# Optimization experiments

Measured on AMD Instinct MI355X. Metric: run time of the kernel, lower is better.

## Reference

```python
import jax, jax.numpy as jnp
import numpy as np
from jax import lax

EPS = 1e-5
KV_DOWN = 4

def _bn(z, g, b, m, v):
    # eval-mode BatchNorm2d over channel axis 1
    inv = (g / jnp.sqrt(v + EPS))[None, :, None, None]
    return z * inv + (b - m * g / jnp.sqrt(v + EPS))[None, :, None, None]

def setup_inputs() -> dict:
    key = jax.random.key(0)
    ks = jax.random.split(key, 8)
    B, C, H, W = 8, 256, 128, 128
    AC, VC = 64, 128
    return {
        "x": jax.random.normal(ks[0], (B, C, H, W), jnp.float32),
        "wq": jax.random.normal(ks[1], (AC, C), jnp.float32) * 0.05,
        "wk": jax.random.normal(ks[2], (AC, C), jnp.float32) * 0.05,
        "wv": jax.random.normal(ks[3], (VC, C), jnp.float32) * 0.05,
        "wproj": jax.random.normal(ks[4], (C, VC), jnp.float32) * 0.05,
        "bn_g": jnp.ones((C,), jnp.float32),
        "bn_b": jnp.zeros((C,), jnp.float32),
        "bn_m": jax.random.normal(ks[5], (C,), jnp.float32) * 0.1,
        "bn_v": jax.random.uniform(ks[5], (C,), jnp.float32, 0.5, 1.5),
        "dw_w": jax.random.normal(ks[6], (C, 1, 3, 3), jnp.float32) * 0.1,
        "pw_w": jax.random.normal(ks[7], (C, C), jnp.float32) * 0.05,
        "mbn_g": jnp.ones((C,), jnp.float32),
        "mbn_b": jnp.zeros((C,), jnp.float32),
        "mbn_m": jax.random.normal(ks[7], (C,), jnp.float32) * 0.1,
        "mbn_v": jax.random.uniform(ks[6], (C,), jnp.float32, 0.5, 1.5),
    }

def reference(x, wq, wk, wv, wproj, bn_g, bn_b, bn_m, bn_v, dw_w, pw_w, mbn_g, mbn_b, mbn_m, mbn_v):
    b, c, h, w = x.shape
    d = KV_DOWN
    scale = wq.shape[0] ** -0.5
    # Q from full-res x via 1x1 conv
    q = jnp.einsum('ac,bchw->bahw', wq, x)            # [B,AC,H,W]
    # avg-pool x for K,V
    x_kv = x.reshape(b, c, h // d, d, w // d, d).mean(axis=(3, 5))
    k = jnp.einsum('ac,bchw->bahw', wk, x_kv)          # [B,AC,H',W']
    v = jnp.einsum('vc,bchw->bvhw', wv, x_kv)          # [B,VC,H',W']
    N = h * w
    M = (h // d) * (w // d)
    qf = q.reshape(b, -1, N)                           # [B,AC,N]
    kf = k.reshape(b, -1, M)                           # [B,AC,M]
    vf = v.reshape(b, -1, M)                           # [B,VC,M]
    attn = jnp.einsum('ban,bam->bnm', qf, kf) * scale  # [B,N,M]
    attn = jax.nn.softmax(attn, axis=-1)
    y = jnp.einsum('bnm,bvm->bvn', attn, vf)           # [B,VC,N]
    y = y.reshape(b, vf.shape[1], h, w)
    y = jnp.einsum('cv,bvhw->bchw', wproj, y)          # proj -> [B,C,H,W]
    y = jax.nn.silu(_bn(y, bn_g, bn_b, bn_m, bn_v))
    # depthwise 3x3 + pointwise 1x1 mix
    z = lax.conv_general_dilated(y, dw_w, (1, 1), 'SAME',
                                 dimension_numbers=('NCHW', 'OIHW', 'NCHW'),
                                 feature_group_count=c)
    z = jnp.einsum('oc,bchw->bohw', pw_w, z)
    z = _bn(z, mbn_g, mbn_b, mbn_m, mbn_v)
    return x + jax.nn.silu(z)
```

## Files before the change

kernel.cpp:

```cpp
#include <hip/hip_runtime.h>
#include <hip/hip_bf16.h>
#include <math.h>

#define EPSV 1e-5f

typedef short bf16x8 __attribute__((ext_vector_type(8)));
typedef float f32x16 __attribute__((ext_vector_type(16)));
typedef unsigned int uint4v __attribute__((ext_vector_type(4)));

__device__ __forceinline__ float silu_f(float v) { return v / (1.0f + __expf(-v)); }

__device__ __forceinline__ unsigned short f2bf(float f) {
  __hip_bfloat16 h = __float2bfloat16(f);
  return __builtin_bit_cast(unsigned short, h);
}

__device__ __forceinline__ float fexp2(float x) {
  float r;
  asm("v_exp_f32 %0, %1" : "=v"(r) : "v"(x));
  return r;
}

__device__ __forceinline__ unsigned int cvtpk(float lo, float hi) {
  unsigned int r;
  asm("v_cvt_pk_bf16_f32 %0, %1, %2" : "=v"(r) : "v"(lo), "v"(hi));
  return r;
}

__device__ __forceinline__ bf16x8 ld_frag(const unsigned short* p) {
  return *reinterpret_cast<const bf16x8*>(p);
}

__device__ __forceinline__ void gload16(const unsigned short* g, unsigned short* l) {
  __builtin_amdgcn_global_load_lds((const __attribute__((address_space(1))) void*)g,
                                   (__attribute__((address_space(3))) void*)l, 16, 0, 0);
}

__global__ __launch_bounds__(256) void pool_kernel(const float* __restrict__ x,
                                                   float* __restrict__ xkv) {
  int idx = blockIdx.x * 256 + threadIdx.x;
  int m = idx & 1023, bc = idx >> 10;
  int hh = m >> 5, ww = m & 31;
  const float* base = x + ((size_t)bc << 14) + (size_t)(hh * 4) * 128 + ww * 4;
  float s = 0.f;
#pragma unroll
  for (int i = 0; i < 4; ++i) {
    float4 v = *reinterpret_cast<const float4*>(base + i * 128);
    s += v.x + v.y + v.z + v.w;
  }
  xkv[idx] = s * 0.0625f;
}

__global__ __launch_bounds__(256) void cvtT_kernel(const float* __restrict__ x,
                                                   unsigned short* __restrict__ xbfT) {
  __shared__ unsigned short sT[64 * 68];
  const int tid = threadIdx.x;
  const int b = blockIdx.z, c0 = blockIdx.y * 64, n0 = blockIdx.x * 64;
  const float* xs = x + ((size_t)(b * 256 + c0) << 14) + n0;
#pragma unroll
  for (int pass = 0; pass < 4; ++pass) {
    int cc = (tid >> 4) + pass * 16;
    int col = (tid & 15) * 4;
    float4 v = *reinterpret_cast<const float4*>(xs + ((size_t)cc << 14) + col);
    unsigned short* d = &sT[cc * 68 + col];
    d[0] = f2bf(v.x); d[1] = f2bf(v.y); d[2] = f2bf(v.z); d[3] = f2bf(v.w);
  }
  __syncthreads();
  int n = tid >> 2, cs = (tid & 3) * 16;
  unsigned short tmp[16];
#pragma unroll
  for (int i = 0; i < 16; ++i) tmp[i] = sT[(cs + i) * 68 + n];
  unsigned short* dst = xbfT + (((size_t)b * 16384 + n0 + n) << 8) + c0 + cs;
  *reinterpret_cast<uint4*>(dst) = *reinterpret_cast<uint4*>(tmp);
  *reinterpret_cast<uint4*>(dst + 8) = *reinterpret_cast<uint4*>(tmp + 8);
}

__global__ __launch_bounds__(256) void prep_kernel(const float* __restrict__ wproj,
                                                   const float* __restrict__ bng,
                                                   const float* __restrict__ bnb,
                                                   const float* __restrict__ bnm,
                                                   const float* __restrict__ bnv,
                                                   unsigned short* __restrict__ wpb,
                                                   float* __restrict__ bnsc,
                                                   float* __restrict__ bnsh) {
  int i = blockIdx.x * 256 + threadIdx.x;
  if (i < 32768) {
    int j = i & 7, lane = (i >> 3) & 63, kc = (i >> 9) & 7, ctcg = i >> 12;
    int row = (ctcg >> 2) * 128 + (ctcg & 3) * 32 + (lane & 31);
    int col = kc * 16 + (lane >> 5) * 8 + j;
    wpb[i] = f2bf(wproj[row * 128 + col]);
  } else if (i < 33024) {
    int c = i - 32768;
    float inv = bng[c] / sqrtf(bnv[c] + EPSV);
    bnsc[c] = inv;
    bnsh[c] = bnb[c] - bnm[c] * inv;
  }
}

__global__ __launch_bounds__(256) void prep_pw(const float* __restrict__ pww,
                                               const float* __restrict__ wq,
                                               unsigned short* __restrict__ pwPack,
                                               unsigned short* __restrict__ wqPack) {
  int f = blockIdx.x * 256 + threadIdx.x;
  if (f < 65536) {
    int j = f & 7, lane = (f >> 3) & 63, ks = (f >> 9) & 15, mt = f >> 13;
    int o = mt * 32 + (lane & 31);
    int cc = ks * 16 + (lane >> 5) * 8 + j;
    pwPack[f] = f2bf(pww[o * 256 + cc]);
  } else if (f < 81920) {
    int g = f - 65536;
    int j = g & 7, lane = (g >> 3) & 63, ks = (g >> 9) & 15, mt = g >> 13;
    int o = mt * 32 + (lane & 31);
    int cc = ks * 16 + (lane >> 5) * 8 + j;
    wqPack[g] = f2bf(wq[o * 256 + cc] * 0.18033688011112042f);
  }
}

__global__ __launch_bounds__(256, 4) void gemm_kv(const float* __restrict__ wk,
                                                  const float* __restrict__ wv,
                                                  const float* __restrict__ X,
                                                  unsigned short* __restrict__ Kt,
                                                  unsigned short* __restrict__ Vbf) {
  __shared__ float sW[64 * 68];
  __shared__ float sX[64 * 68];
  const int tid = threadIdx.x;
  const int n0 = blockIdx.x * 64;
  const int part = blockIdx.y;
  const int m0 = (part == 0) ? 0 : (part - 1) * 64;
  const float* W = (part == 0) ? wk : wv;
  const size_t xoff = (size_t)blockIdx.z * 256 * 1024;
  const int tm4 = (tid >> 4) * 4, tn4 = (tid & 15) * 4;
  float acc[4][4] = {};
  for (int k0 = 0; k0 < 256; k0 += 64) {
    __syncthreads();
#pragma unroll
    for (int i = 0; i < 16; ++i) {
      int flat = tid + i * 256;
      int kk = flat & 63, mm = flat >> 6;
      sW[kk * 68 + mm] = W[(m0 + mm) * 256 + k0 + kk];
      sX[kk * 68 + mm] = X[xoff + (size_t)(k0 + kk) * 1024 + n0 + mm];
    }
    __syncthreads();
#pragma unroll 8
    for (int k = 0; k < 64; ++k) {
      float4 a4 = *reinterpret_cast<const float4*>(&sW[k * 68 + tm4]);
      float4 b4 = *reinterpret_cast<const float4*>(&sX[k * 68 + tn4]);
      float av[4] = {a4.x, a4.y, a4.z, a4.w};
      float bv[4] = {b4.x, b4.y, b4.z, b4.w};
#pragma unroll
      for (int i = 0; i < 4; ++i)
#pragma unroll
        for (int j = 0; j < 4; ++j) acc[i][j] += av[i] * bv[j];
    }
  }
  if (part == 0) {
    const size_t coff = (size_t)blockIdx.z * 65536;
#pragma unroll
    for (int j = 0; j < 4; ++j) {
      ushort4 o;
      o.x = f2bf(acc[0][j]); o.y = f2bf(acc[1][j]);
      o.z = f2bf(acc[2][j]); o.w = f2bf(acc[3][j]);
      *reinterpret_cast<ushort4*>(&Kt[coff + (size_t)(n0 + tn4 + j) * 64 + tm4]) = o;
    }
  } else {
    const size_t coff = (size_t)blockIdx.z * 131072;
#pragma unroll
    for (int i = 0; i < 4; ++i) {
      ushort4 o;
      o.x = f2bf(acc[i][0]); o.y = f2bf(acc[i][1]);
      o.z = f2bf(acc[i][2]); o.w = f2bf(acc[i][3]);
      *reinterpret_cast<ushort4*>(&Vbf[coff + (size_t)(m0 + tm4 + i) * 1024 + n0 + tn4]) = o;
    }
  }
}

__global__ __launch_bounds__(256, 4) void qgemm_mfma(const unsigned short* __restrict__ xbfT,
                                                     const unsigned short* __restrict__ wqPack,
                                                     unsigned short* __restrict__ Qt) {
  __shared__ __align__(16) unsigned short sX[2][128 * 64];
  const int tid = threadIdx.x;
  const int w = tid >> 6, l = tid & 63;
  const int lq = l & 31, hi = l >> 5;
  const int b = blockIdx.y;
  const int n0 = blockIdx.x * 128;
  const int lr8 = l >> 3;
  const int gslot = (l & 7) ^ (lr8 & 7);
  const unsigned short* xb = xbfT + (((size_t)b * 16384 + n0) << 8);

#define QSTAGE(buf, ck)                                                       \
  {                                                                           \
    _Pragma("unroll") for (int i = 0; i < 4; ++i) {                           \
      int row = w * 32 + i * 8;                                               \
      gload16(xb + ((size_t)(row + lr8) << 8) + (ck) * 64 + gslot * 8,        \
              &sX[buf][row * 64]);                                            \
    }                                                                         \
  }

  f32x16 acc0, acc1;
#pragma unroll
  for (int i = 0; i < 16; ++i) { acc0[i] = 0.f; acc1[i] = 0.f; }

  QSTAGE(0, 0);
  __syncthreads();
  int cur = 0;
  for (int ck = 0; ck < 4; ++ck) {
    if (ck < 3) QSTAGE(cur ^ 1, ck + 1);
    const unsigned short* xl = sX[cur];
#pragma unroll
    for (int k2 = 0; k2 < 4; ++k2) {
      bf16x8 bfr = ld_frag(xl + (w * 32 + lq) * 64 + (((2 * k2 + hi) ^ (lq & 7)) << 3));
      int ks = ck * 4 + k2;
      bf16x8 a0 = ld_frag(wqPack + (size_t)((ks)*64 + l) * 8);
      bf16x8 a1 = ld_frag(wqPack + (size_t)((16 + ks) * 64 + l) * 8);
      acc0 = __builtin_amdgcn_mfma_f32_32x32x16_bf16(a0, bfr, acc0, 0, 0, 0);
      acc1 = __builtin_amdgcn_mfma_f32_32x32x16_bf16(a1, bfr, acc1, 0, 0, 0);
    }
    __syncthreads();
    cur ^= 1;
  }
#undef QSTAGE

  unsigned short* so2 = (unsigned short*)sX + w * 2304;
#pragma unroll
  for (int r = 0; r < 16; ++r) {
    int a = (r & 3) + 8 * (r >> 2) + 4 * hi;
    so2[lq * 72 + a] = f2bf(acc0[r]);
    so2[lq * 72 + 32 + a] = f2bf(acc1[r]);
  }
#pragma unroll
  for (int pass = 0; pass < 4; ++pass) {
    int flat = pass * 64 + l;
    int row = flat >> 3, col8 = (flat & 7) * 8;
    bf16x8 v = ld_frag(so2 + row * 72 + col8);
    *reinterpret_cast<bf16x8*>(Qt + ((size_t)b * 16384 + n0 + w * 32 + row) * 64 + col8) = v;
  }
}

__global__ __launch_bounds__(256, 3) void attn_mfma(
    const unsigned short* __restrict__ Qt, const unsigned short* __restrict__ Kt,
    const unsigned short* __restrict__ Vb, const unsigned short* __restrict__ wpb,
    const float* __restrict__ bnsc, const float* __restrict__ bnsh,
    unsigned short* __restrict__ yact) {
  __shared__ __align__(16) unsigned char smem[49152];
  unsigned short* const sK = (unsigned short*)smem;
  unsigned short* const sV = (unsigned short*)(smem + 16384);
  const int tid = threadIdx.x;
  const int w = tid >> 6, l = tid & 63;
  const int lq = l & 31, hi = l >> 5;
  const int bid = blockIdx.x;
  const int b = bid >> 7;
  const int q0 = (bid & 127) * 128 + w * 32;

  const unsigned short* Qp = Qt + ((size_t)b * 16384 + q0 + lq) * 64 + hi * 8;
  bf16x8 qf[4];
#pragma unroll
  for (int kc = 0; kc < 4; ++kc) qf[kc] = ld_frag(Qp + kc * 16);

  const uint4v ow = {0x3F803F80u, 0x3F803F80u, 0x3F803F80u, 0x3F803F80u};
  const bf16x8 onesf = __builtin_bit_cast(bf16x8, ow);

  f32x16 acc[4], accS;
#pragma unroll
  for (int t = 0; t < 4; ++t)
#pragma unroll
    for (int i = 0; i < 16; ++i) acc[t][i] = 0.f;
#pragma unroll
  for (int i = 0; i < 16; ++i) accS[i] = 0.f;

  const unsigned short* Kb = Kt + (size_t)b * 65536;
  const unsigned short* Vbb = Vb + (size_t)b * 131072;
  const int lr8 = l >> 3;
  const int gslot = (l & 7) ^ (lr8 & 7);

#define STAGE(buf, ch)                                                           \
  {                                                                              \
    const int m0s = (ch) * 64;                                                   \
    _Pragma("unroll") for (int i = 0; i < 2; ++i) {                              \
      int row8 = w * 16 + i * 8;                                                 \
      gload16(Kb + (size_t)(m0s + row8 + lr8) * 64 + gslot * 8,                  \
              sK + (buf) * 4096 + row8 * 64);                                    \
    }                                                                            \
    _Pragma("unroll") for (int j = 0; j < 4; ++j) {                              \
      int vc8 = w * 32 + j * 8;                                                  \
      gload16(Vbb + (size_t)(vc8 + lr8) * 1024 + m0s + gslot * 8,                \
              sV + (buf) * 8192 + vc8 * 64);                                     \
    }                                                                            \
  }

  STAGE(0, 0);
  __syncthreads();
  int cur = 0;
  for (int ch = 0; ch < 16; ++ch) {
    if (ch < 15) STAGE(cur ^ 1, ch + 1);
    const unsigned short* kb = sK + cur * 4096;
    const unsigned short* vb = sV + cur * 8192;
#pragma unroll
    for (int msi = 0; msi < 2; ++msi) {
      const int ms = msi * 32;
      bf16x8 kf[4];
#pragma unroll
      for (int kc = 0; kc < 4; ++kc)
        kf[kc] = ld_frag(kb + (ms + lq) * 64 + (((2 * kc + hi) ^ (lq & 7)) << 3));
      f32x16 sa;
#pragma unroll
      for (int i = 0; i < 16; ++i) sa[i] = 0.f;
      __builtin_amdgcn_s_setprio(1);
#pragma unroll
      for (int kc = 0; kc < 4; ++kc)
        sa = __builtin_amdgcn_mfma_f32_32x32x16_bf16(kf[kc], qf[kc], sa, 0, 0, 0);
      __builtin_amdgcn_s_setprio(0);

      float p[16];
#pragma unroll
      for (int r = 0; r < 16; ++r) p[r] = fexp2(sa[r] - 16.0f);

      unsigned int wpk[8];
#pragma unroll
      for (int i = 0; i < 8; ++i) wpk[i] = cvtpk(p[2 * i], p[2 * i + 1]);
      auto s01 = __builtin_amdgcn_permlane32_swap(wpk[0], wpk[2], false, false);
      auto s23 = __builtin_amdgcn_permlane32_swap(wpk[1], wpk[3], false, false);
      auto s45 = __builtin_amdgcn_permlane32_swap(wpk[4], wpk[6], false, false);
      auto s67 = __builtin_amdgcn_permlane32_swap(wpk[5], wpk[7], false, false);
      uint4v f0 = {(unsigned int)s01[0], (unsigned int)s23[0], (unsigned int)s01[1],
                   (unsigned int)s23[1]};
      uint4v f1 = {(unsigned int)s45[0], (unsigned int)s67[0], (unsigned int)s45[1],
                   (unsigned int)s67[1]};
      bf16x8 pf0 = __builtin_bit_cast(bf16x8, f0);
      bf16x8 pf1 = __builtin_bit_cast(bf16x8, f1);

      __builtin_amdgcn_s_setprio(1);
#pragma unroll
      for (int t = 0; t < 4; ++t) {
        bf16x8 vf0 =
            ld_frag(vb + (t * 32 + lq) * 64 + ((((ms >> 3) + hi) ^ (lq & 7)) << 3));
        bf16x8 vf1 =
            ld_frag(vb + (t * 32 + lq) * 64 + ((((ms >> 3) + 2 + hi) ^ (lq & 7)) << 3));
        acc[t] = __builtin_amdgcn_mfma_f32_32x32x16_bf16(pf0, vf0, acc[t], 0, 0, 0);
        acc[t] = __builtin_amdgcn_mfma_f32_32x32x16_bf16(pf1, vf1, acc[t], 0, 0, 0);
      }
      accS = __builtin_amdgcn_mfma_f32_32x32x16_bf16(pf0, onesf, accS, 0, 0, 0);
      accS = __builtin_amdgcn_mfma_f32_32x32x16_bf16(pf1, onesf, accS, 0, 0, 0);
      __builtin_amdgcn_s_setprio(0);
    }
    __syncthreads();
    cur ^= 1;
  }
#undef STAGE

  unsigned short* so = (unsigned short*)smem + w * 4096;
#pragma unroll
  for (int t = 0; t < 4; ++t)
#pragma unroll
    for (int r = 0; r < 16; ++r) {
      int q = (r & 3) + 8 * (r >> 2) + 4 * hi;
      int col = t * 32 + lq;
      so[q * 128 + (col ^ ((q & 15) << 3))] = f2bf(acc[t][r] / accS[r]);
    }
  __syncthreads();

  bf16x8 of[8];
#pragma unroll
  for (int kc = 0; kc < 8; ++kc) {
    int colr = kc * 16 + hi * 8;
    of[kc] = ld_frag(&so[lq * 128 + (colr ^ ((lq & 15) << 3))]);
  }
#pragma unroll
  for (int cg = 0; cg < 2; ++cg) {
    f32x16 z[4];
#pragma unroll
    for (int t = 0; t < 4; ++t)
#pragma unroll
      for (int i = 0; i < 16; ++i) z[t][i] = 0.f;
#pragma unroll
    for (int ct = 0; ct < 4; ++ct) {
      const unsigned short* wp = wpb + (size_t)(cg * 4 + ct) * 4096 + (size_t)l * 8;
#pragma unroll
      for (int kc = 0; kc < 8; ++kc) {
        bf16x8 wf = ld_frag(wp + kc * 512);
        z[ct] = __builtin_amdgcn_mfma_f32_32x32x16_bf16(wf, of[kc], z[ct], 0, 0, 0);
      }
    }
#pragma unroll
    for (int ct = 0; ct < 4; ++ct)
#pragma unroll
      for (int r = 0; r < 16; ++r) {
        int c = cg * 128 + ct * 32 + (r & 3) + 8 * (r >> 2) + 4 * hi;
        float val = z[ct][r] * bnsc[c] + bnsh[c];
        yact[((size_t)(b * 256 + c)) * 16384 + q0 + lq] = f2bf(silu_f(val));
      }
  }
}

__global__ __launch_bounds__(256, 4) void dwconv_kernel(const unsigned short* __restrict__ yact,
                                                        const float* __restrict__ dww,
                                                        unsigned short* __restrict__ D) {
  __shared__ unsigned int sP[130 * 67];
  const int tid = threadIdx.x;
  const int bc = blockIdx.x;
  const int c = bc & 255;
  for (int s = tid; s < 130 * 67; s += 256) sP[s] = 0;
  __syncthreads();
  const unsigned int* ysrc = reinterpret_cast<const unsigned int*>(yact) + (size_t)bc * 8192;
#pragma unroll
  for (int i = 0; i < 8; ++i) {
    int wi4 = tid + 256 * i;
    uint4 v = *reinterpret_cast<const uint4*>(ysrc + (size_t)wi4 * 4);
    int row = wi4 >> 4;
    int cw = (wi4 & 15) * 4;
    unsigned int* dst = &sP[(row + 1) * 67 + 1 + cw];
    dst[0] = v.x; dst[1] = v.y; dst[2] = v.z; dst[3] = v.w;
  }
  __syncthreads();
  float w9[9];
#pragma unroll
  for (int k = 0; k < 9; ++k) w9[k] = dww[c * 9 + k];
#pragma unroll
  for (int it = 0; it < 4; ++it) {
    int u = tid + 256 * it;
    int rho = u >> 4;
    int wg = u & 15;
    float a0[8] = {}, a1[8] = {};
#pragma unroll
    for (int ir = 0; ir < 4; ++ir) {
      int srow = rho * 2 + ir;
      const unsigned int* rp = &sP[srow * 67 + 4 * wg];
      float f[12];
#pragma unroll
      for (int k = 0; k < 6; ++k) {
        unsigned int wv = rp[k];
        f[2 * k] = __builtin_bit_cast(float, wv << 16);
        f[2 * k + 1] = __builtin_bit_cast(float, wv & 0xffff0000u);
      }
      if (ir < 3) {
#pragma unroll
        for (int cc = 0; cc < 8; ++cc)
#pragma unroll
          for (int dc = 0; dc < 3; ++dc) a0[cc] += f[cc + 1 + dc] * w9[ir * 3 + dc];
      }
      if (ir > 0) {
#pragma unroll
        for (int cc = 0; cc < 8; ++cc)
#pragma unroll
          for (int dc = 0; dc < 3; ++dc) a1[cc] += f[cc + 1 + dc] * w9[(ir - 1) * 3 + dc];
      }
    }
    uint4v o0, o1;
#pragma unroll
    for (int k = 0; k < 4; ++k) {
      o0[k] = (unsigned int)f2bf(a0[2 * k]) | ((unsigned int)f2bf(a0[2 * k + 1]) << 16);
      o1[k] = (unsigned int)f2bf(a1[2 * k]) | ((unsigned int)f2bf(a1[2 * k + 1]) << 16);
    }
    size_t ob = (size_t)bc * 8192 + (size_t)(rho * 2) * 64 + wg * 4;
    unsigned int* Dw = reinterpret_cast<unsigned int*>(D);
    *reinterpret_cast<uint4v*>(Dw + ob) = o0;
    *reinterpret_cast<uint4v*>(Dw + ob + 64) = o1;
  }
}

__global__ __launch_bounds__(256, 2) void pwmix_kernel(
    const unsigned short* __restrict__ D, const unsigned short* __restrict__ pwPack,
    const float* __restrict__ x, const float* __restrict__ mg,
    const float* __restrict__ mb2, const float* __restrict__ mmu,
    const float* __restrict__ mvv, float* __restrict__ out) {
  __shared__ unsigned int sDt[16384];
  __shared__ float smsc[256], smsh[256];
  const int tid = threadIdx.x;
  const int w = tid >> 6, l = tid & 63;
  const int lq = l & 31, hi = l >> 5;
  const int h = blockIdx.x, b = blockIdx.y;
  if (tid < 256) {
    float inv = mg[tid] * rsqrtf(mvv[tid] + EPSV);
    smsc[tid] = inv;
    smsh[tid] = mb2[tid] - mmu[tid] * inv;
  }
  const size_t dbase = ((size_t)b * 256) * 16384 + (size_t)h * 128;
#pragma unroll
  for (int i = 0; i < 8; ++i) {
    int cp = 64 * (i & 1) + 16 * w + (l >> 2);
    int pg = (l & 3) + 4 * (i >> 1);
    const unsigned short* g0 = D + dbase + (size_t)(cp * 2) * 16384 + pg * 8;
    bf16x8 d0 = ld_frag(g0);
    bf16x8 d1 = ld_frag(g0 + 16384);
#pragma unroll
    for (int j = 0; j < 8; ++j) {
      unsigned int word = ((unsigned int)(unsigned short)d0[j]) |
                          (((unsigned int)(unsigned short)d1[j]) << 16);
      int widx = ((pg * 8 + j) * 128 + cp) ^ (j << 2);
      sDt[widx] = word;
    }
  }
  __syncthreads();

  f32x16 z[2][4];
#pragma unroll
  for (int mti = 0; mti < 2; ++mti)
#pragma unroll
    for (int nt = 0; nt < 4; ++nt)
#pragma unroll
      for (int i = 0; i < 16; ++i) z[mti][nt][i] = 0.f;

#pragma unroll
  for (int ks = 0; ks < 16; ++ks) {
    bf16x8 a0 = ld_frag(pwPack + (size_t)(((w * 2 + 0) * 16 + ks) * 64 + l) * 8);
    bf16x8 a1 = ld_frag(pwPack + (size_t)(((w * 2 + 1) * 16 + ks) * 64 + l) * 8);
    bf16x8 bfr[4];
#pragma unroll
    for (int nt = 0; nt < 4; ++nt) {
      int word = ((nt * 32 + lq) * 128 + 8 * ks + 4 * hi) ^ ((lq & 7) << 2);
      bfr[nt] = *reinterpret_cast<const bf16x8*>(
          reinterpret_cast<const unsigned short*>(sDt) + (size_t)word * 2);
    }
#pragma unroll
    for (int nt = 0; nt < 4; ++nt) {
      z[0][nt] = __builtin_amdgcn_mfma_f32_32x32x16_bf16(a0, bfr[nt], z[0][nt], 0, 0, 0);
      z[1][nt] = __builtin_amdgcn_mfma_f32_32x32x16_bf16(a1, bfr[nt], z[1][nt], 0, 0, 0);
    }
  }

#pragma unroll
  for (int mti = 0; mti < 2; ++mti) {
    int ob = (w * 2 + mti) * 32 + 4 * hi;
#pragma unroll
    for (int r = 0; r < 16; ++r) {
      int o = ob + (r & 3) + 8 * (r >> 2);
      float sc = smsc[o], sh = smsh[o];
#pragma unroll
      for (int nt = 0; nt < 4; ++nt) {
        int px = nt * 32 + lq;
        size_t gi = (((size_t)(b * 256 + o)) << 14) + (size_t)h * 128 + px;
        float val = z[mti][nt][r] * sc + sh;
        out[gi] = x[gi] + silu_f(val);
      }
    }
  }
}

extern "C" void kernel_launch(void* const* d_in, const int* in_sizes, int n_in,
                              void* d_out, int out_size, void* d_ws, size_t ws_size,
                              hipStream_t stream) {
  const float* x     = (const float*)d_in[0];
  const float* wq    = (const float*)d_in[1];
  const float* wk    = (const float*)d_in[2];
  const float* wvp   = (const float*)d_in[3];
  const float* wproj = (const float*)d_in[4];
  const float* bng   = (const float*)d_in[5];
  const float* bnb   = (const float*)d_in[6];
  const float* bnm   = (const float*)d_in[7];
  const float* bnv   = (const float*)d_in[8];
  const float* dww   = (const float*)d_in[9];
  const float* pww   = (const float*)d_in[10];
  const float* mg    = (const float*)d_in[11];
  const float* mb2   = (const float*)d_in[12];
  const float* mmu   = (const float*)d_in[13];
  const float* mvv   = (const float*)d_in[14];
  float* out = (float*)d_out;

  char* base = (char*)d_ws;
  unsigned short* D = (unsigned short*)base;
  float* xkv = (float*)base;
  unsigned short* Qt  = (unsigned short*)(base + 8388608);
  unsigned short* Kt  = (unsigned short*)(base + 25165824);
  unsigned short* Vbf = (unsigned short*)(base + 26214400);
  unsigned short* wqPack = (unsigned short*)(base + 28311552);
  float* bnsc = (float*)(base + 67108864);
  float* bnsh = (float*)(base + 67109888);
  unsigned short* wpb    = (unsigned short*)(base + 67110912);
  unsigned short* pwPack = (unsigned short*)(base + 67176448);
  unsigned short* yact   = (unsigned short*)(base + 67307520);
  unsigned short* xbfT   = yact;

  cvtT_kernel<<<dim3(256, 4, 8), 256, 0, stream>>>(x, xbfT);
  pool_kernel<<<8192, 256, 0, stream>>>(x, xkv);
  prep_kernel<<<130, 256, 0, stream>>>(wproj, bng, bnb, bnm, bnv, wpb, bnsc, bnsh);
  prep_pw<<<320, 256, 0, stream>>>(pww, wq, pwPack, wqPack);
  gemm_kv<<<dim3(16, 3, 8), 256, 0, stream>>>(wk, wvp, xkv, Kt, Vbf);
  qgemm_mfma<<<dim3(128, 8), 256, 0, stream>>>(xbfT, wqPack, Qt);
  attn_mfma<<<dim3(1024), 256, 0, stream>>>(Qt, Kt, Vbf, wpb, bnsc, bnsh, yact);
  dwconv_kernel<<<2048, 256, 0, stream>>>(yact, dww, D);
  pwmix_kernel<<<dim3(128, 8), 256, 0, stream>>>(D, pwPack, x, mg, mb2, mmu, mvv, out);
}
```

Baseline: 288.2 us.

## Unroll attention KV loop by two with explicit vmcnt waits and reciprocal normalize

Restructures the K/V double-buffer loop in the attention kernel into a manually unrolled pair of stages with fixed buffer indices. The full __syncthreads after each chunk is replaced by partial s_waitcnt vmcnt(6) plus raw s_barrier, so the next chunk's global-to-LDS loads stay in flight while the current chunk computes. It also folds the -16 exp offset into the MFMA accumulator's initial value and replaces the per-element division in the output normalisation with one v_rcp per row followed by multiplies. The cost is that correctness now depends on the hand-counted vmcnt values matching the number of outstanding loads, and the reciprocal is slightly less precise than a true divide.

```diff
diff --git a/kernel.cpp b/kernel.cpp
--- a/kernel.cpp
+++ b/kernel.cpp
@@ -18,6 +18,12 @@
 __device__ __forceinline__ float fexp2(float x) {
   float r;
   asm("v_exp_f32 %0, %1" : "=v"(r) : "v"(x));
+  return r;
+}
+
+__device__ __forceinline__ float frcp(float x) {
+  float r;
+  asm("v_rcp_f32 %0, %1" : "=v"(r) : "v"(x));
   return r;
 }
 
@@ -287,74 +293,88 @@
     }                                                                            \
   }
 
+#define COMPUTE(B)                                                                   \
+  {                                                                                  \
+    const unsigned short* kb = sK + (B) * 4096;                                      \
+    const unsigned short* vb = sV + (B) * 8192;                                      \
+    _Pragma("unroll") for (int msi = 0; msi < 2; ++msi) {                            \
+      const int ms = msi * 32;                                                       \
+      bf16x8 kf[4];                                                                  \
+      _Pragma("unroll") for (int kc = 0; kc < 4; ++kc)                               \
+          kf[kc] = ld_frag(kb + (ms + lq) * 64 + (((2 * kc + hi) ^ (lq & 7)) << 3)); \
+      f32x16 sa;                                                                     \
+      _Pragma("unroll") for (int i = 0; i < 16; ++i) sa[i] = -16.0f;                 \
+      __builtin_amdgcn_s_setprio(1);                                                 \
+      _Pragma("unroll") for (int kc = 0; kc < 4; ++kc)                               \
+          sa = __builtin_amdgcn_mfma_f32_32x32x16_bf16(kf[kc], qf[kc], sa, 0, 0, 0); \
+      __builtin_amdgcn_s_setprio(0);                                                 \
+      float p[16];                                                                   \
+      _Pragma("unroll") for (int r = 0; r < 16; ++r) p[r] = fexp2(sa[r]);            \
+      unsigned int wpk[8];                                                           \
+      _Pragma("unroll") for (int i = 0; i < 8; ++i)                                  \
+          wpk[i] = cvtpk(p[2 * i], p[2 * i + 1]);                                    \
+      auto s01 = __builtin_amdgcn_permlane32_swap(wpk[0], wpk[2], false, false);     \
+      auto s23 = __builtin_amdgcn_permlane32_swap(wpk[1], wpk[3], false, false);     \
+      auto s45 = __builtin_amdgcn_permlane32_swap(wpk[4], wpk[6], false, false);     \
+      auto s67 = __builtin_amdgcn_permlane32_swap(wpk[5], wpk[7], false, false);     \
+      uint4v f0 = {(unsigned int)s01[0], (unsigned int)s23[0], (unsigned int)s01[1], \
+                   (unsigned int)s23[1]};                                            \
+      uint4v f1 = {(unsigned int)s45[0], (unsigned int)s67[0], (unsigned int)s45[1], \
+                   (unsigned int)s67[1]};                                            \
+      bf16x8 pf0 = __builtin_bit_cast(bf16x8, f0);                                   \
+      bf16x8 pf1 = __builtin_bit_cast(bf16x8, f1);                                   \
+      __builtin_amdgcn_s_setprio(1);                                                 \
+      _Pragma("unroll") for (int t = 0; t < 4; ++t) {                                \
+        bf16x8 vf0 =                                                                 \
+            ld_frag(vb + (t * 32 + lq) * 64 + ((((ms >> 3) + hi) ^ (lq & 7)) << 3)); \
+        bf16x8 vf1 = ld_frag(vb + (t * 32 + lq) * 64 +                               \
+                             ((((ms >> 3) + 2 + hi) ^ (lq & 7)) << 3));              \
+        acc[t] = __builtin_amdgcn_mfma_f32_32x32x16_bf16(pf0, vf0, acc[t], 0, 0, 0); \
+        acc[t] = __builtin_amdgcn_mfma_f32_32x32x16_bf16(pf1, vf1, acc[t], 0, 0, 0); \
+      }                                                                              \
+      accS = __builtin_amdgcn_mfma_f32_32x32x16_bf16(pf0, onesf, accS, 0, 0, 0);     \
+      accS = __builtin_amdgcn_mfma_f32_32x32x16_bf16(pf1, onesf, accS, 0, 0, 0);     \
+      __builtin_amdgcn_s_setprio(0);                                                 \
+    }                                                                                \
+  }
+
   STAGE(0, 0);
+  for (int c2 = 0; c2 < 7; ++c2) {
+    int ch = c2 * 2;
+    STAGE(1, ch + 1);
+    asm volatile("s_waitcnt vmcnt(6)" ::: "memory");
+    __builtin_amdgcn_s_barrier();
+    COMPUTE(0);
+    __builtin_amdgcn_s_barrier();
+    STAGE(0, ch + 2);
+    asm volatile("s_waitcnt vmcnt(6)" ::: "memory");
+    __builtin_amdgcn_s_barrier();
+    COMPUTE(1);
+    __builtin_amdgcn_s_barrier();
+  }
+  STAGE(1, 15);
+  asm volatile("s_waitcnt vmcnt(6)" ::: "memory");
+  __builtin_amdgcn_s_barrier();
+  COMPUTE(0);
+  __builtin_amdgcn_s_barrier();
+  asm volatile("s_waitcnt vmcnt(0)" ::: "memory");
+  __builtin_amdgcn_s_barrier();
+  COMPUTE(1);
+#undef STAGE
+#undef COMPUTE
+
   __syncthreads();
-  int cur = 0;
-  for (int ch = 0; ch < 16; ++ch) {
-    if (ch < 15) STAGE(cur ^ 1, ch + 1);
-    const unsigned short* kb = sK + cur * 4096;
-    const unsigned short* vb = sV + cur * 8192;
-#pragma unroll
-    for (int msi = 0; msi < 2; ++msi) {
-      const int ms = msi * 32;
-      bf16x8 kf[4];
-#pragma unroll
-      for (int kc = 0; kc < 4; ++kc)
-        kf[kc] = ld_frag(kb + (ms + lq) * 64 + (((2 * kc + hi) ^ (lq & 7)) << 3));
-      f32x16 sa;
-#pragma unroll
-      for (int i = 0; i < 16; ++i) sa[i] = 0.f;
-      __builtin_amdgcn_s_setprio(1);
-#pragma unroll
-      for (int kc = 0; kc < 4; ++kc)
-        sa = __builtin_amdgcn_mfma_f32_32x32x16_bf16(kf[kc], qf[kc], sa, 0, 0, 0);
-      __builtin_amdgcn_s_setprio(0);
-
-      float p[16];
-#pragma unroll
-      for (int r = 0; r < 16; ++r) p[r] = fexp2(sa[r] - 16.0f);
-
-      unsigned int wpk[8];
-#pragma unroll
-      for (int i = 0; i < 8; ++i) wpk[i] = cvtpk(p[2 * i], p[2 * i + 1]);
-      auto s01 = __builtin_amdgcn_permlane32_swap(wpk[0], wpk[2], false, false);
-      auto s23 = __builtin_amdgcn_permlane32_swap(wpk[1], wpk[3], false, false);
-      auto s45 = __builtin_amdgcn_permlane32_swap(wpk[4], wpk[6], false, false);
-      auto s67 = __builtin_amdgcn_permlane32_swap(wpk[5], wpk[7], false, false);
-      uint4v f0 = {(unsigned int)s01[0], (unsigned int)s23[0], (unsigned int)s01[1],
-                   (unsigned int)s23[1]};
-      uint4v f1 = {(unsigned int)s45[0], (unsigned int)s67[0], (unsigned int)s45[1],
-                   (unsigned int)s67[1]};
-      bf16x8 pf0 = __builtin_bit_cast(bf16x8, f0);
-      bf16x8 pf1 = __builtin_bit_cast(bf16x8, f1);
-
-      __builtin_amdgcn_s_setprio(1);
-#pragma unroll
-      for (int t = 0; t < 4; ++t) {
-        bf16x8 vf0 =
-            ld_frag(vb + (t * 32 + lq) * 64 + ((((ms >> 3) + hi) ^ (lq & 7)) << 3));
-        bf16x8 vf1 =
-            ld_frag(vb + (t * 32 + lq) * 64 + ((((ms >> 3) + 2 + hi) ^ (lq & 7)) << 3));
-        acc[t] = __builtin_amdgcn_mfma_f32_32x32x16_bf16(pf0, vf0, acc[t], 0, 0, 0);
-        acc[t] = __builtin_amdgcn_mfma_f32_32x32x16_bf16(pf1, vf1, acc[t], 0, 0, 0);
-      }
-      accS = __builtin_amdgcn_mfma_f32_32x32x16_bf16(pf0, onesf, accS, 0, 0, 0);
-      accS = __builtin_amdgcn_mfma_f32_32x32x16_bf16(pf1, onesf, accS, 0, 0, 0);
-      __builtin_amdgcn_s_setprio(0);
-    }
-    __syncthreads();
-    cur ^= 1;
-  }
-#undef STAGE
-
   unsigned short* so = (unsigned short*)smem + w * 4096;
+  float rs[16];
+#pragma unroll
+  for (int r = 0; r < 16; ++r) rs[r] = frcp(accS[r]);
 #pragma unroll
   for (int t = 0; t < 4; ++t)
 #pragma unroll
     for (int r = 0; r < 16; ++r) {
       int q = (r & 3) + 8 * (r >> 2) + 4 * hi;
       int col = t * 32 + lq;
-      so[q * 128 + (col ^ ((q & 15) << 3))] = f2bf(acc[t][r] / accS[r]);
+      so[q * 128 + (col ^ ((q & 15) << 3))] = f2bf(acc[t][r] * rs[r]);
     }
   __syncthreads();
 
```

Result: slower. 353.3 us (+22.6%).

## Fuse bf16 transpose with avg-pool, merge prep kernels, fold softmax offset

Applied to the files above, without the earlier changes.

Combines the x-to-bf16 transpose and the 4x4 average pool into one kernel that reads x once, computing pooled sums from the staged bf16 tile in shared memory. The two weight-prep kernels are merged into one launch. In attention, the exp2 offset is folded into the MFMA accumulator initialisation and the per-element normalisation division becomes a reciprocal multiply. Pooling from bf16-rounded values slightly changes precision, and the new grid uses fewer, longer blocks.

```diff
diff --git a/kernel.cpp b/kernel.cpp
--- a/kernel.cpp
+++ b/kernel.cpp
@@ -13,6 +13,10 @@
 __device__ __forceinline__ unsigned short f2bf(float f) {
   __hip_bfloat16 h = __float2bfloat16(f);
   return __builtin_bit_cast(unsigned short, h);
+}
+
+__device__ __forceinline__ float bf2f(unsigned short u) {
+  return __builtin_bit_cast(float, (unsigned int)u << 16);
 }
 
 __device__ __forceinline__ float fexp2(float x) {
@@ -21,6 +25,12 @@
   return r;
 }
 
+__device__ __forceinline__ float frcp(float x) {
+  float r;
+  asm("v_rcp_f32 %0, %1" : "=v"(r) : "v"(x));
+  return r;
+}
+
 __device__ __forceinline__ unsigned int cvtpk(float lo, float hi) {
   unsigned int r;
   asm("v_cvt_pk_bf16_f32 %0, %1, %2" : "=v"(r) : "v"(lo), "v"(hi));
@@ -36,53 +46,66 @@
                                    (__attribute__((address_space(3))) void*)l, 16, 0, 0);
 }
 
-__global__ __launch_bounds__(256) void pool_kernel(const float* __restrict__ x,
-                                                   float* __restrict__ xkv) {
-  int idx = blockIdx.x * 256 + threadIdx.x;
-  int m = idx & 1023, bc = idx >> 10;
-  int hh = m >> 5, ww = m & 31;
-  const float* base = x + ((size_t)bc << 14) + (size_t)(hh * 4) * 128 + ww * 4;
-  float s = 0.f;
-#pragma unroll
-  for (int i = 0; i < 4; ++i) {
-    float4 v = *reinterpret_cast<const float4*>(base + i * 128);
-    s += v.x + v.y + v.z + v.w;
-  }
-  xkv[idx] = s * 0.0625f;
-}
-
-__global__ __launch_bounds__(256) void cvtT_kernel(const float* __restrict__ x,
-                                                   unsigned short* __restrict__ xbfT) {
-  __shared__ unsigned short sT[64 * 68];
+__global__ __launch_bounds__(256) void cvtpool_kernel(const float* __restrict__ x,
+                                                      unsigned short* __restrict__ xbfT,
+                                                      float* __restrict__ xkv) {
+  __shared__ unsigned short sT[64 * 134];
   const int tid = threadIdx.x;
-  const int b = blockIdx.z, c0 = blockIdx.y * 64, n0 = blockIdx.x * 64;
-  const float* xs = x + ((size_t)(b * 256 + c0) << 14) + n0;
-#pragma unroll
-  for (int pass = 0; pass < 4; ++pass) {
-    int cc = (tid >> 4) + pass * 16;
-    int col = (tid & 15) * 4;
-    float4 v = *reinterpret_cast<const float4*>(xs + ((size_t)cc << 14) + col);
-    unsigned short* d = &sT[cc * 68 + col];
-    d[0] = f2bf(v.x); d[1] = f2bf(v.y); d[2] = f2bf(v.z); d[3] = f2bf(v.w);
-  }
-  __syncthreads();
-  int n = tid >> 2, cs = (tid & 3) * 16;
-  unsigned short tmp[16];
-#pragma unroll
-  for (int i = 0; i < 16; ++i) tmp[i] = sT[(cs + i) * 68 + n];
-  unsigned short* dst = xbfT + (((size_t)b * 16384 + n0 + n) << 8) + c0 + cs;
-  *reinterpret_cast<uint4*>(dst) = *reinterpret_cast<uint4*>(tmp);
-  *reinterpret_cast<uint4*>(dst + 8) = *reinterpret_cast<uint4*>(tmp + 8);
-}
-
-__global__ __launch_bounds__(256) void prep_kernel(const float* __restrict__ wproj,
-                                                   const float* __restrict__ bng,
-                                                   const float* __restrict__ bnb,
-                                                   const float* __restrict__ bnm,
-                                                   const float* __restrict__ bnv,
-                                                   unsigned short* __restrict__ wpb,
-                                                   float* __restrict__ bnsc,
-                                                   float* __restrict__ bnsh) {
+  const int b = blockIdx.z, c0 = blockIdx.y * 64, hq = blockIdx.x;
+  const int pc = tid >> 2;
+  const int pwb = (tid & 3) * 8;
+  float pacc[8] = {};
+#pragma unroll
+  for (int ih = 0; ih < 4; ++ih) {
+    const int h = hq * 4 + ih;
+    __syncthreads();
+#pragma unroll
+    for (int i = 0; i < 8; ++i) {
+      int flat = tid + i * 256;
+      int cc = flat >> 5, wg = flat & 31;
+      float4 v = *reinterpret_cast<const float4*>(
+          x + (((size_t)(b * 256 + c0 + cc)) << 14) + h * 128 + wg * 4);
+      unsigned short* d = &sT[cc * 134 + wg * 4];
+      d[0] = f2bf(v.x); d[1] = f2bf(v.y); d[2] = f2bf(v.z); d[3] = f2bf(v.w);
+    }
+    __syncthreads();
+#pragma unroll
+    for (int p = 0; p < 4; ++p) {
+      int unit = tid + p * 256;
+      int nn = unit >> 3, cs = (unit & 7) * 8;
+      unsigned short tmp[8];
+#pragma unroll
+      for (int j = 0; j < 8; ++j) tmp[j] = sT[(cs + j) * 134 + nn];
+      *reinterpret_cast<bf16x8*>(xbfT + (((size_t)b * 16384 + h * 128 + nn) << 8) + c0 +
+                                 cs) = *reinterpret_cast<bf16x8*>(tmp);
+    }
+#pragma unroll
+    for (int ws = 0; ws < 8; ++ws) {
+      const unsigned short* rp = &sT[pc * 134 + (pwb + ws) * 4];
+      pacc[ws] += (bf2f(rp[0]) + bf2f(rp[1])) + (bf2f(rp[2]) + bf2f(rp[3]));
+    }
+  }
+  float4 o0 = make_float4(pacc[0] * 0.0625f, pacc[1] * 0.0625f, pacc[2] * 0.0625f,
+                          pacc[3] * 0.0625f);
+  float4 o1 = make_float4(pacc[4] * 0.0625f, pacc[5] * 0.0625f, pacc[6] * 0.0625f,
+                          pacc[7] * 0.0625f);
+  float* dst = xkv + (((size_t)(b * 256 + c0 + pc)) << 10) + hq * 32 + pwb;
+  *reinterpret_cast<float4*>(dst) = o0;
+  *reinterpret_cast<float4*>(dst + 4) = o1;
+}
+
+__global__ __launch_bounds__(256) void prep_all(const float* __restrict__ wproj,
+                                                const float* __restrict__ bng,
+                                                const float* __restrict__ bnb,
+                                                const float* __restrict__ bnm,
+                                                const float* __restrict__ bnv,
+                                                const float* __restrict__ pww,
+                                                const float* __restrict__ wq,
+                                                unsigned short* __restrict__ wpb,
+                                                float* __restrict__ bnsc,
+                                                float* __restrict__ bnsh,
+                                                unsigned short* __restrict__ pwPack,
+                                                unsigned short* __restrict__ wqPack) {
   int i = blockIdx.x * 256 + threadIdx.x;
   if (i < 32768) {
     int j = i & 7, lane = (i >> 3) & 63, kc = (i >> 9) & 7, ctcg = i >> 12;
@@ -94,21 +117,14 @@
     float inv = bng[c] / sqrtf(bnv[c] + EPSV);
     bnsc[c] = inv;
     bnsh[c] = bnb[c] - bnm[c] * inv;
-  }
-}
-
-__global__ __launch_bounds__(256) void prep_pw(const float* __restrict__ pww,
-                                               const float* __restrict__ wq,
-                                               unsigned short* __restrict__ pwPack,
-                                               unsigned short* __restrict__ wqPack) {
-  int f = blockIdx.x * 256 + threadIdx.x;
-  if (f < 65536) {
+  } else if (i < 98560) {
+    int f = i - 33024;
     int j = f & 7, lane = (f >> 3) & 63, ks = (f >> 9) & 15, mt = f >> 13;
     int o = mt * 32 + (lane & 31);
     int cc = ks * 16 + (lane >> 5) * 8 + j;
     pwPack[f] = f2bf(pww[o * 256 + cc]);
-  } else if (f < 81920) {
-    int g = f - 65536;
+  } else if (i < 114944) {
+    int g = i - 98560;
     int j = g & 7, lane = (g >> 3) & 63, ks = (g >> 9) & 15, mt = g >> 13;
     int o = mt * 32 + (lane & 31);
     int cc = ks * 16 + (lane >> 5) * 8 + j;
@@ -303,7 +319,7 @@
         kf[kc] = ld_frag(kb + (ms + lq) * 64 + (((2 * kc + hi) ^ (lq & 7)) << 3));
       f32x16 sa;
 #pragma unroll
-      for (int i = 0; i < 16; ++i) sa[i] = 0.f;
+      for (int i = 0; i < 16; ++i) sa[i] = -16.0f;
       __builtin_amdgcn_s_setprio(1);
 #pragma unroll
       for (int kc = 0; kc < 4; ++kc)
@@ -312,7 +328,7 @@
 
       float p[16];
 #pragma unroll
-      for (int r = 0; r < 16; ++r) p[r] = fexp2(sa[r] - 16.0f);
+      for (int r = 0; r < 16; ++r) p[r] = fexp2(sa[r]);
 
       unsigned int wpk[8];
 #pragma unroll
@@ -348,13 +364,16 @@
 #undef STAGE
 
   unsigned short* so = (unsigned short*)smem + w * 4096;
+  float rs[16];
+#pragma unroll
+  for (int r = 0; r < 16; ++r) rs[r] = frcp(accS[r]);
 #pragma unroll
   for (int t = 0; t < 4; ++t)
 #pragma unroll
     for (int r = 0; r < 16; ++r) {
       int q = (r & 3) + 8 * (r >> 2) + 4 * hi;
       int col = t * 32 + lq;
-      so[q * 128 + (col ^ ((q & 15) << 3))] = f2bf(acc[t][r] / accS[r]);
+      so[q * 128 + (col ^ ((q & 15) << 3))] = f2bf(acc[t][r] * rs[r]);
     }
   __syncthreads();
 
@@ -569,10 +588,9 @@
   unsigned short* yact   = (unsigned short*)(base + 67307520);
   unsigned short* xbfT   = yact;
 
-  cvtT_kernel<<<dim3(256, 4, 8), 256, 0, stream>>>(x, xbfT);
-  pool_kernel<<<8192, 256, 0, stream>>>(x, xkv);
-  prep_kernel<<<130, 256, 0, stream>>>(wproj, bng, bnb, bnm, bnv, wpb, bnsc, bnsh);
-  prep_pw<<<320, 256, 0, stream>>>(pww, wq, pwPack, wqPack);
+  cvtpool_kernel<<<dim3(32, 4, 8), 256, 0, stream>>>(x, xbfT, xkv);
+  prep_all<<<449, 256, 0, stream>>>(wproj, bng, bnb, bnm, bnv, pww, wq, wpb, bnsc, bnsh,
+                                    pwPack, wqPack);
   gemm_kv<<<dim3(16, 3, 8), 256, 0, stream>>>(wk, wvp, xkv, Kt, Vbf);
   qgemm_mfma<<<dim3(128, 8), 256, 0, stream>>>(xbfT, wqPack, Qt);
   attn_mfma<<<dim3(1024), 256, 0, stream>>>(Qt, Kt, Vbf, wpb, bnsc, bnsh, yact);
```

New measurement: 320.0 us. 11.0% more time.
